# Kernel optimization log

Measured on AMD Instinct MI355X. Metric: run time of the kernel, lower is better.

Reference implementation:

```python
import jax, jax.numpy as jnp
import numpy as np

N_NODES = 100000
N_EDGES = 1600000
NODE_DIM = 64
EDGE_DIM = 32
HIDDEN = 64
LN_EPS = 1e-5


def _leaky_relu(x):
    return jnp.where(x >= 0, x, 0.1 * x)


def setup_inputs() -> dict:
    key = jax.random.key(0)
    ks = jax.random.split(key, 12)
    inp = {
        "node_features": jax.random.normal(ks[0], (N_NODES, NODE_DIM), dtype=jnp.float32),
        "edge_index": jax.random.randint(ks[1], (2, N_EDGES), 0, N_NODES, dtype=jnp.int32),
        "edge_attr": jax.random.normal(ks[2], (N_EDGES, EDGE_DIM), dtype=jnp.float32),
        "edge_weights": jax.random.uniform(ks[3], (N_EDGES,), dtype=jnp.float32),
        # message_mlp: Linear(node+edge -> hidden), LeakyReLU(0.1), Linear(hidden -> node)
        "mW1": jax.random.normal(ks[4], (NODE_DIM + EDGE_DIM, HIDDEN), dtype=jnp.float32) * 0.1,
        "mb1": jnp.zeros((HIDDEN,), dtype=jnp.float32),
        "mW2": jax.random.normal(ks[5], (HIDDEN, NODE_DIM), dtype=jnp.float32) * 0.1,
        "mb2": jnp.zeros((NODE_DIM,), dtype=jnp.float32),
        # update_mlp: Linear(2*node -> hidden), LayerNorm(hidden), LeakyReLU(0.1), Linear(hidden -> node)
        "uW1": jax.random.normal(ks[6], (2 * NODE_DIM, HIDDEN), dtype=jnp.float32) * 0.1,
        "ub1": jnp.zeros((HIDDEN,), dtype=jnp.float32),
        "ln_g": jnp.ones((HIDDEN,), dtype=jnp.float32),
        "ln_b": jnp.zeros((HIDDEN,), dtype=jnp.float32),
        "uW2": jax.random.normal(ks[7], (HIDDEN, NODE_DIM), dtype=jnp.float32) * 0.1,
        "ub2": jnp.zeros((NODE_DIM,), dtype=jnp.float32),
    }
    return inp


def reference(node_features, edge_index, edge_attr, edge_weights,
              mW1, mb1, mW2, mb2, uW1, ub1, ln_g, ln_b, uW2, ub2):
    src_idx, dst_idx = edge_index[0], edge_index[1]
    src_features = node_features[src_idx]                    # [E, node_dim] gather
    msg_input = jnp.concatenate([src_features, edge_attr], axis=-1)  # [E, node+edge]
    h = _leaky_relu(msg_input @ mW1 + mb1)                    # [E, hidden]
    messages = (h @ mW2 + mb2) * edge_weights[:, None]        # [E, node_dim]
    aggregated = jax.ops.segment_sum(messages, dst_idx, num_segments=node_features.shape[0])
    combined = jnp.concatenate([node_features, aggregated], axis=-1)  # [N, 2*node_dim]
    z = combined @ uW1 + ub1                                  # [N, hidden]
    mu = jnp.mean(z, axis=-1, keepdims=True)
    var = jnp.mean((z - mu) ** 2, axis=-1, keepdims=True)
    z = (z - mu) * jax.lax.rsqrt(var + LN_EPS) * ln_g + ln_b
    z = _leaky_relu(z)
    return z @ uW2 + ub2                                      # [N, node_dim]
```

## Files before the change

kernel.cpp:

```cpp
#include <hip/hip_runtime.h>
#include <cstdint>
#include <cstddef>

#define NN 100000
#define NE 1600000

typedef __attribute__((ext_vector_type(8))) short bf16x8;
typedef __attribute__((ext_vector_type(4))) short bf16x4;
typedef __attribute__((ext_vector_type(4))) float f32x4;

__device__ __forceinline__ short f2bf(float f) {
  uint32_t u = __builtin_bit_cast(uint32_t, f);
  u += 0x7FFFu + ((u >> 16) & 1u);
  return (short)(u >> 16);
}

__device__ __forceinline__ float lrelu(float x) { return fmaxf(x, 0.1f * x); }

__device__ __forceinline__ void atomic_add_f32(float* p, float v) {
  __hip_atomic_fetch_add(p, v, __ATOMIC_RELAXED, __HIP_MEMORY_SCOPE_AGENT);
}

__global__ void prep_kernel(const float* __restrict__ W1, const float* __restrict__ W2,
                            const float* __restrict__ uW1, const float* __restrict__ uW2,
                            short* __restrict__ ws) {
  int t = blockIdx.x * 256 + threadIdx.x;
  const int n1 = 64 * 96, n2 = 64 * 64, n3 = 64 * 128, n4 = 64 * 64;
  if (t < n1) { int c = t / 96, k = t % 96; ws[t] = f2bf(W1[k * 64 + c]); return; }
  t -= n1;
  if (t < n2) { int c = t / 64, k = t % 64; ws[n1 + t] = f2bf(W2[k * 64 + c]); return; }
  t -= n2;
  if (t < n3) { int c = t / 128, k = t % 128; ws[n1 + n2 + t] = f2bf(uW1[k * 64 + c]); return; }
  t -= n3;
  if (t < n4) { int c = t / 64, k = t % 64; ws[n1 + n2 + n3 + t] = f2bf(uW2[k * 64 + c]); return; }
}

__global__ __launch_bounds__(256) void edge_kernel(
    const float* __restrict__ nf, const int* __restrict__ ei,
    const float* __restrict__ ea, const float* __restrict__ ew,
    const short* __restrict__ W1t, const float* __restrict__ b1,
    const short* __restrict__ W2t, const float* __restrict__ b2,
    float* __restrict__ agg) {
  __shared__ uint4 hbuf_s[4][512];
  const int tid = threadIdx.x;
  const int wv = tid >> 6, ln = tid & 63;
  const int c = ln & 15, g = ln >> 4;
  char* hb = (char*)hbuf_s[wv];
  const long base = ((long)blockIdx.x * 4 + wv) * 64;

  int eid[4], srcn[4];
#pragma unroll
  for (int n = 0; n < 4; ++n) {
    eid[n] = (int)base + 16 * n + c;
    srcn[n] = ei[eid[n]];
  }

  f32x4 acc1[4][4];
#pragma unroll
  for (int i = 0; i < 4; ++i)
#pragma unroll
    for (int j = 0; j < 4; ++j) acc1[i][j] = f32x4{0.f, 0.f, 0.f, 0.f};

#pragma unroll
  for (int ks = 0; ks < 3; ++ks) {
    bf16x8 xf[4];
#pragma unroll
    for (int n = 0; n < 4; ++n) {
      const float* p = (ks < 2) ? (nf + (size_t)srcn[n] * 64 + ks * 32 + g * 8)
                                : (ea + (size_t)eid[n] * 32 + g * 8);
      float4 u = *(const float4*)p;
      float4 v = *(const float4*)(p + 4);
      bf16x8 t;
      t[0] = f2bf(u.x); t[1] = f2bf(u.y); t[2] = f2bf(u.z); t[3] = f2bf(u.w);
      t[4] = f2bf(v.x); t[5] = f2bf(v.y); t[6] = f2bf(v.z); t[7] = f2bf(v.w);
      xf[n] = t;
    }
#pragma unroll
    for (int m = 0; m < 4; ++m) {
      bf16x8 wf = *(const bf16x8*)(W1t + (size_t)(16 * m + c) * 96 + ks * 32 + g * 8);
#pragma unroll
      for (int n = 0; n < 4; ++n)
        acc1[m][n] = __builtin_amdgcn_mfma_f32_16x16x32_bf16(wf, xf[n], acc1[m][n], 0, 0, 0);
    }
  }

  float b1v[4][4];
#pragma unroll
  for (int m = 0; m < 4; ++m)
#pragma unroll
    for (int r = 0; r < 4; ++r) b1v[m][r] = b1[16 * m + 4 * g + r];

#pragma unroll
  for (int m = 0; m < 4; ++m) {
    const int h0 = 16 * m + 4 * g;
#pragma unroll
    for (int n = 0; n < 4; ++n) {
      const int e = 16 * n + c;
      bf16x4 pk;
#pragma unroll
      for (int r = 0; r < 4; ++r) pk[r] = f2bf(lrelu(acc1[m][n][r] + b1v[m][r]));
      const int byte = e * 128 + ((h0 * 2) ^ ((e & 7) << 4));
      *(bf16x4*)(hb + byte) = pk;
    }
  }

  f32x4 acc2[4][4];
#pragma unroll
  for (int i = 0; i < 4; ++i)
#pragma unroll
    for (int j = 0; j < 4; ++j) acc2[i][j] = f32x4{0.f, 0.f, 0.f, 0.f};

#pragma unroll
  for (int ks = 0; ks < 2; ++ks) {
    bf16x8 hf[4];
#pragma unroll
    for (int m = 0; m < 4; ++m) {
      const int e = 16 * m + c;
      const int byte = e * 128 + ((ks * 64 + g * 16) ^ ((e & 7) << 4));
      hf[m] = *(const bf16x8*)(hb + byte);
    }
#pragma unroll
    for (int n = 0; n < 4; ++n) {
      bf16x8 wf = *(const bf16x8*)(W2t + (size_t)(16 * n + c) * 64 + ks * 32 + g * 8);
#pragma unroll
      for (int m = 0; m < 4; ++m)
        acc2[m][n] = __builtin_amdgcn_mfma_f32_16x16x32_bf16(hf[m], wf, acc2[m][n], 0, 0, 0);
    }
  }

  float b2v[4];
#pragma unroll
  for (int n = 0; n < 4; ++n) b2v[n] = b2[16 * n + c];

#pragma unroll
  for (int m = 0; m < 4; ++m) {
#pragma unroll
    for (int r = 0; r < 4; ++r) {
      const long e = base + 16 * m + 4 * g + r;
      const float w = ew[e];
      const int dst = ei[NE + e];
      float* ab = agg + (size_t)dst * 64 + c;
#pragma unroll
      for (int n = 0; n < 4; ++n)
        atomic_add_f32(ab + 16 * n, (acc2[m][n][r] + b2v[n]) * w);
    }
  }
}

__global__ __launch_bounds__(256) void node_kernel(
    const float* __restrict__ nf,
    const short* __restrict__ W1t, const float* __restrict__ b1,
    const float* __restrict__ gam, const float* __restrict__ bet,
    const short* __restrict__ W2t, const float* __restrict__ b2,
    float* __restrict__ io) {
  __shared__ uint4 hbuf_s[4][512];
  const int tid = threadIdx.x;
  const int wv = tid >> 6, ln = tid & 63;
  const int c = ln & 15, g = ln >> 4;
  char* hb = (char*)hbuf_s[wv];
  const long base = ((long)blockIdx.x * 4 + wv) * 64;

  int nid[4];
#pragma unroll
  for (int n = 0; n < 4; ++n) {
    long r = base + 16 * n + c;
    nid[n] = (r < NN) ? (int)r : (NN - 1);
  }

  f32x4 acc1[4][4];
#pragma unroll
  for (int i = 0; i < 4; ++i)
#pragma unroll
    for (int j = 0; j < 4; ++j) acc1[i][j] = f32x4{0.f, 0.f, 0.f, 0.f};

#pragma unroll
  for (int ks = 0; ks < 4; ++ks) {
    bf16x8 xf[4];
#pragma unroll
    for (int n = 0; n < 4; ++n) {
      const float* p = (ks < 2) ? (nf + (size_t)nid[n] * 64 + ks * 32 + g * 8)
                                : (io + (size_t)nid[n] * 64 + (ks - 2) * 32 + g * 8);
      float4 u = *(const float4*)p;
      float4 v = *(const float4*)(p + 4);
      bf16x8 t;
      t[0] = f2bf(u.x); t[1] = f2bf(u.y); t[2] = f2bf(u.z); t[3] = f2bf(u.w);
      t[4] = f2bf(v.x); t[5] = f2bf(v.y); t[6] = f2bf(v.z); t[7] = f2bf(v.w);
      xf[n] = t;
    }
#pragma unroll
    for (int m = 0; m < 4; ++m) {
      bf16x8 wf = *(const bf16x8*)(W1t + (size_t)(16 * m + c) * 128 + ks * 32 + g * 8);
#pragma unroll
      for (int n = 0; n < 4; ++n)
        acc1[m][n] = __builtin_amdgcn_mfma_f32_16x16x32_bf16(wf, xf[n], acc1[m][n], 0, 0, 0);
    }
  }

  float b1v[4][4], gv[4][4], bv[4][4];
#pragma unroll
  for (int m = 0; m < 4; ++m)
#pragma unroll
    for (int r = 0; r < 4; ++r) {
      int h = 16 * m + 4 * g + r;
      b1v[m][r] = b1[h]; gv[m][r] = gam[h]; bv[m][r] = bet[h];
    }

#pragma unroll
  for (int n = 0; n < 4; ++n) {
    float s = 0.f;
#pragma unroll
    for (int m = 0; m < 4; ++m)
#pragma unroll
      for (int r = 0; r < 4; ++r) { acc1[m][n][r] += b1v[m][r]; s += acc1[m][n][r]; }
    s += __shfl_xor(s, 16);
    s += __shfl_xor(s, 32);
    const float mu = s * 0.015625f;
    float vs = 0.f;
#pragma unroll
    for (int m = 0; m < 4; ++m)
#pragma unroll
      for (int r = 0; r < 4; ++r) { float d = acc1[m][n][r] - mu; vs += d * d; }
    vs += __shfl_xor(vs, 16);
    vs += __shfl_xor(vs, 32);
    const float rstd = rsqrtf(vs * 0.015625f + 1e-5f);
    const int e = 16 * n + c;
#pragma unroll
    for (int m = 0; m < 4; ++m) {
      bf16x4 pk;
#pragma unroll
      for (int r = 0; r < 4; ++r)
        pk[r] = f2bf(lrelu((acc1[m][n][r] - mu) * rstd * gv[m][r] + bv[m][r]));
      const int byte = e * 128 + (((16 * m + 4 * g) * 2) ^ ((e & 7) << 4));
      *(bf16x4*)(hb + byte) = pk;
    }
  }

  f32x4 acc2[4][4];
#pragma unroll
  for (int i = 0; i < 4; ++i)
#pragma unroll
    for (int j = 0; j < 4; ++j) acc2[i][j] = f32x4{0.f, 0.f, 0.f, 0.f};

#pragma unroll
  for (int ks = 0; ks < 2; ++ks) {
    bf16x8 hf[4];
#pragma unroll
    for (int m = 0; m < 4; ++m) {
      const int e = 16 * m + c;
      const int byte = e * 128 + ((ks * 64 + g * 16) ^ ((e & 7) << 4));
      hf[m] = *(const bf16x8*)(hb + byte);
    }
#pragma unroll
    for (int n = 0; n < 4; ++n) {
      bf16x8 wf = *(const bf16x8*)(W2t + (size_t)(16 * n + c) * 64 + ks * 32 + g * 8);
#pragma unroll
      for (int m = 0; m < 4; ++m)
        acc2[m][n] = __builtin_amdgcn_mfma_f32_16x16x32_bf16(hf[m], wf, acc2[m][n], 0, 0, 0);
    }
  }

  float b2v[4];
#pragma unroll
  for (int n = 0; n < 4; ++n) b2v[n] = b2[16 * n + c];

#pragma unroll
  for (int m = 0; m < 4; ++m)
#pragma unroll
    for (int r = 0; r < 4; ++r) {
      const long node = base + 16 * m + 4 * g + r;
      if (node < NN) {
        float* op = io + (size_t)node * 64 + c;
#pragma unroll
        for (int n = 0; n < 4; ++n) op[16 * n] = acc2[m][n][r] + b2v[n];
      }
    }
}

extern "C" void kernel_launch(void* const* d_in, const int* in_sizes, int n_in,
                              void* d_out, int out_size, void* d_ws, size_t ws_size,
                              hipStream_t stream) {
  const float* nf  = (const float*)d_in[0];
  const int*   ei  = (const int*)d_in[1];
  const float* ea  = (const float*)d_in[2];
  const float* ew  = (const float*)d_in[3];
  const float* mW1 = (const float*)d_in[4];
  const float* mb1 = (const float*)d_in[5];
  const float* mW2 = (const float*)d_in[6];
  const float* mb2 = (const float*)d_in[7];
  const float* uW1 = (const float*)d_in[8];
  const float* ub1 = (const float*)d_in[9];
  const float* lng = (const float*)d_in[10];
  const float* lnb = (const float*)d_in[11];
  const float* uW2 = (const float*)d_in[12];
  const float* ub2 = (const float*)d_in[13];
  float* io = (float*)d_out;
  short* wsw = (short*)d_ws;

  hipMemsetAsync(d_out, 0, (size_t)NN * 64 * sizeof(float), stream);
  prep_kernel<<<88, 256, 0, stream>>>(mW1, mW2, uW1, uW2, wsw);

  const short* W1t  = wsw;
  const short* W2t  = wsw + 64 * 96;
  const short* uW1t = wsw + 64 * 96 + 64 * 64;
  const short* uW2t = uW1t + 64 * 128;

  edge_kernel<<<NE / 256, 256, 0, stream>>>(nf, ei, ea, ew, W1t, mb1, W2t, mb2, io);
  node_kernel<<<(NN + 255) / 256, 256, 0, stream>>>(nf, uW1t, ub1, lng, lnb, uW2t, ub2, io);
}
```

Baseline: 391.3 us.

## Sort edges by destination (CSR) and fuse edge MLP, aggregation and node update

Builds a destination-sorted edge list each call with a histogram, a two-level scan and an atomic scatter. A single fused kernel then processes 64 destination nodes per block: it runs the message MLP over that block's edges, accumulates into shared memory with LDS atomics instead of global atomics, and applies the update MLP with LayerNorm directly from shared memory. This removes the global atomic traffic, the output memset and the round trip of the aggregate through global memory. In exchange it adds several sort kernels and scattered writes, causes load imbalance across blocks with varying edge counts, and falls back to the old path if the workspace is too small.

New measurement: 950.6 us. +142.9%, slower.

```diff
diff --git a/kernel.cpp b/kernel.cpp
--- a/kernel.cpp
+++ b/kernel.cpp
@@ -4,10 +4,20 @@
 
 #define NN 100000
 #define NE 1600000
+#define NB ((NN + 63) / 64)
 
 typedef __attribute__((ext_vector_type(8))) short bf16x8;
 typedef __attribute__((ext_vector_type(4))) short bf16x4;
 typedef __attribute__((ext_vector_type(4))) float f32x4;
+
+#define OFF_W    0u
+#define OFF_CNT  45056u
+#define OFF_OFF  445056u
+#define OFF_CUR  845120u
+#define OFF_BS   1245120u
+#define OFF_SE   1245632u
+#define OFF_SD   14045632u
+#define WS_NEED  20445632u
 
 __device__ __forceinline__ short f2bf(float f) {
   uint32_t u = __builtin_bit_cast(uint32_t, f);
@@ -35,6 +45,300 @@
   if (t < n4) { int c = t / 64, k = t % 64; ws[n1 + n2 + n3 + t] = f2bf(uW2[k * 64 + c]); return; }
 }
 
+__global__ __launch_bounds__(256) void hist_kernel(const int* __restrict__ ei,
+                                                   int* __restrict__ cnt) {
+  int t = blockIdx.x * 256 + threadIdx.x;
+  if (t < NE) atomicAdd(&cnt[ei[NE + t]], 1);
+}
+
+__global__ __launch_bounds__(1024) void scan_block_kernel(const int* __restrict__ cnt,
+                                                          int* __restrict__ off,
+                                                          int* __restrict__ bs) {
+  __shared__ int wsum[16];
+  const int tid = threadIdx.x, lane = tid & 63, w = tid >> 6;
+  const int i = blockIdx.x * 1024 + tid;
+  int v = (i < NN) ? cnt[i] : 0;
+  int x = v;
+#pragma unroll
+  for (int d = 1; d < 64; d <<= 1) { int t = __shfl_up(x, d); if (lane >= d) x += t; }
+  if (lane == 63) wsum[w] = x;
+  __syncthreads();
+  if (w == 0) {
+    int s = (lane < 16) ? wsum[lane] : 0;
+#pragma unroll
+    for (int d = 1; d < 16; d <<= 1) { int t = __shfl_up(s, d); if (lane >= d) s += t; }
+    if (lane < 16) wsum[lane] = s;
+  }
+  __syncthreads();
+  int incl = x + ((w > 0) ? wsum[w - 1] : 0);
+  if (i < NN) off[i] = incl - v;
+  if (tid == 1023) bs[blockIdx.x] = incl;
+}
+
+__global__ __launch_bounds__(1024) void scan_add_kernel(int* __restrict__ off,
+                                                        const int* __restrict__ bs,
+                                                        int* __restrict__ cur) {
+  __shared__ int sbase;
+  const int tid = threadIdx.x, cB = blockIdx.x;
+  if (tid < 64) {
+    int s = 0;
+    if (tid < cB && tid < 98) s += bs[tid];
+    int j2 = tid + 64;
+    if (j2 < cB && j2 < 98) s += bs[j2];
+#pragma unroll
+    for (int d = 1; d < 64; d <<= 1) s += __shfl_xor(s, d);
+    if (tid == 0) sbase = s;
+  }
+  __syncthreads();
+  const int base = sbase;
+  const int i = cB * 1024 + tid;
+  if (i < NN) { int o = off[i] + base; off[i] = o; cur[i] = o; }
+}
+
+__global__ __launch_bounds__(256) void scatter_kernel(const int* __restrict__ ei,
+                                                      int* __restrict__ cur,
+                                                      int2* __restrict__ sse,
+                                                      int* __restrict__ sdst) {
+  int t = blockIdx.x * 256 + threadIdx.x;
+  if (t >= NE) return;
+  int d = ei[NE + t];
+  int pos = atomicAdd(&cur[d], 1);
+  sse[pos] = make_int2(ei[t], t);
+  sdst[pos] = d;
+}
+
+__global__ __launch_bounds__(256) void fused_kernel(
+    const float* __restrict__ nf, const float* __restrict__ ea,
+    const float* __restrict__ ew,
+    const int2* __restrict__ sse, const int* __restrict__ sdst,
+    const int* __restrict__ off,
+    const short* __restrict__ W1t, const float* __restrict__ b1,
+    const short* __restrict__ W2t, const float* __restrict__ b2,
+    const short* __restrict__ uW1t, const float* __restrict__ ub1,
+    const float* __restrict__ gam, const float* __restrict__ bet,
+    const short* __restrict__ uW2t, const float* __restrict__ ub2,
+    float* __restrict__ out) {
+  __shared__ float sAgg[64 * 68];
+  __shared__ uint4 hbuf_s[4][512];
+  __shared__ int   tdst[4][64];
+  __shared__ float tw[4][64];
+
+  const int tid = threadIdx.x;
+  const int wv = tid >> 6, ln = tid & 63;
+  const int c = ln & 15, g = ln >> 4;
+  char* hb = (char*)hbuf_s[wv];
+  const int nb = blockIdx.x * 64;
+
+  for (int i = tid; i < 64 * 68; i += 256) sAgg[i] = 0.f;
+
+  const int e0 = off[nb];
+  const int nhi = nb + 64;
+  const int e1 = (nhi >= NN) ? NE : off[nhi];
+  __syncthreads();
+
+  float b1v[4][4];
+#pragma unroll
+  for (int m = 0; m < 4; ++m)
+#pragma unroll
+    for (int r = 0; r < 4; ++r) b1v[m][r] = b1[16 * m + 4 * g + r];
+  float b2v[4];
+#pragma unroll
+  for (int n = 0; n < 4; ++n) b2v[n] = b2[16 * n + c];
+
+  for (int t0 = e0 + wv * 64; t0 < e1; t0 += 256) {
+    int src[4], eid[4];
+#pragma unroll
+    for (int n = 0; n < 4; ++n) {
+      int slot = t0 + 16 * n + c;
+      bool val = slot < e1;
+      int2 se = val ? sse[slot] : make_int2(0, 0);
+      src[n] = se.x; eid[n] = se.y;
+      if (g == 0) {
+        tdst[wv][16 * n + c] = val ? (sdst[slot] - nb) : 0;
+        tw[wv][16 * n + c]   = val ? ew[se.y] : 0.f;
+      }
+    }
+
+    f32x4 acc1[4][4];
+#pragma unroll
+    for (int i = 0; i < 4; ++i)
+#pragma unroll
+      for (int j = 0; j < 4; ++j) acc1[i][j] = f32x4{0.f, 0.f, 0.f, 0.f};
+
+#pragma unroll
+    for (int ks = 0; ks < 3; ++ks) {
+      bf16x8 xf[4];
+#pragma unroll
+      for (int n = 0; n < 4; ++n) {
+        const float* p = (ks < 2) ? (nf + (size_t)src[n] * 64 + ks * 32 + g * 8)
+                                  : (ea + (size_t)eid[n] * 32 + g * 8);
+        float4 u = *(const float4*)p;
+        float4 v = *(const float4*)(p + 4);
+        bf16x8 t;
+        t[0] = f2bf(u.x); t[1] = f2bf(u.y); t[2] = f2bf(u.z); t[3] = f2bf(u.w);
+        t[4] = f2bf(v.x); t[5] = f2bf(v.y); t[6] = f2bf(v.z); t[7] = f2bf(v.w);
+        xf[n] = t;
+      }
+#pragma unroll
+      for (int m = 0; m < 4; ++m) {
+        bf16x8 wf = *(const bf16x8*)(W1t + (size_t)(16 * m + c) * 96 + ks * 32 + g * 8);
+#pragma unroll
+        for (int n = 0; n < 4; ++n)
+          acc1[m][n] = __builtin_amdgcn_mfma_f32_16x16x32_bf16(wf, xf[n], acc1[m][n], 0, 0, 0);
+      }
+    }
+
+#pragma unroll
+    for (int m = 0; m < 4; ++m) {
+      const int h0 = 16 * m + 4 * g;
+#pragma unroll
+      for (int n = 0; n < 4; ++n) {
+        const int e = 16 * n + c;
+        bf16x4 pk;
+#pragma unroll
+        for (int r = 0; r < 4; ++r) pk[r] = f2bf(lrelu(acc1[m][n][r] + b1v[m][r]));
+        const int byte = e * 128 + ((h0 * 2) ^ ((e & 7) << 4));
+        *(bf16x4*)(hb + byte) = pk;
+      }
+    }
+
+    f32x4 acc2[4][4];
+#pragma unroll
+    for (int i = 0; i < 4; ++i)
+#pragma unroll
+      for (int j = 0; j < 4; ++j) acc2[i][j] = f32x4{0.f, 0.f, 0.f, 0.f};
+
+#pragma unroll
+    for (int ks = 0; ks < 2; ++ks) {
+      bf16x8 hf[4];
+#pragma unroll
+      for (int m = 0; m < 4; ++m) {
+        const int e = 16 * m + c;
+        const int byte = e * 128 + ((ks * 64 + g * 16) ^ ((e & 7) << 4));
+        hf[m] = *(const bf16x8*)(hb + byte);
+      }
+#pragma unroll
+      for (int n = 0; n < 4; ++n) {
+        bf16x8 wf = *(const bf16x8*)(W2t + (size_t)(16 * n + c) * 64 + ks * 32 + g * 8);
+#pragma unroll
+        for (int m = 0; m < 4; ++m)
+          acc2[m][n] = __builtin_amdgcn_mfma_f32_16x16x32_bf16(hf[m], wf, acc2[m][n], 0, 0, 0);
+      }
+    }
+
+#pragma unroll
+    for (int m = 0; m < 4; ++m)
+#pragma unroll
+      for (int r = 0; r < 4; ++r) {
+        const int s2 = 16 * m + 4 * g + r;
+        const int dl = tdst[wv][s2];
+        const float w = tw[wv][s2];
+#pragma unroll
+        for (int n = 0; n < 4; ++n)
+          atomicAdd(&sAgg[dl * 68 + c + 16 * n], (acc2[m][n][r] + b2v[n]) * w);
+      }
+  }
+  __syncthreads();
+
+  const int nloc = 16 * wv + c;
+  const int nodec = nb + nloc;
+  const int ncl = (nodec < NN) ? nodec : (NN - 1);
+
+  f32x4 un[4];
+#pragma unroll
+  for (int m = 0; m < 4; ++m) un[m] = f32x4{0.f, 0.f, 0.f, 0.f};
+
+#pragma unroll
+  for (int ks = 0; ks < 4; ++ks) {
+    bf16x8 xf;
+    float4 u, v;
+    if (ks < 2) {
+      const float* p = nf + (size_t)ncl * 64 + ks * 32 + g * 8;
+      u = *(const float4*)p; v = *(const float4*)(p + 4);
+    } else {
+      const float* p = sAgg + nloc * 68 + (ks - 2) * 32 + g * 8;
+      u = *(const float4*)p; v = *(const float4*)(p + 4);
+    }
+    xf[0] = f2bf(u.x); xf[1] = f2bf(u.y); xf[2] = f2bf(u.z); xf[3] = f2bf(u.w);
+    xf[4] = f2bf(v.x); xf[5] = f2bf(v.y); xf[6] = f2bf(v.z); xf[7] = f2bf(v.w);
+#pragma unroll
+    for (int m = 0; m < 4; ++m) {
+      bf16x8 wf = *(const bf16x8*)(uW1t + (size_t)(16 * m + c) * 128 + ks * 32 + g * 8);
+      un[m] = __builtin_amdgcn_mfma_f32_16x16x32_bf16(wf, xf, un[m], 0, 0, 0);
+    }
+  }
+
+  float b1n[4][4], gn[4][4], bn[4][4];
+#pragma unroll
+  for (int m = 0; m < 4; ++m)
+#pragma unroll
+    for (int r = 0; r < 4; ++r) {
+      int h = 16 * m + 4 * g + r;
+      b1n[m][r] = ub1[h]; gn[m][r] = gam[h]; bn[m][r] = bet[h];
+    }
+
+  float s = 0.f;
+#pragma unroll
+  for (int m = 0; m < 4; ++m)
+#pragma unroll
+    for (int r = 0; r < 4; ++r) { un[m][r] += b1n[m][r]; s += un[m][r]; }
+  s += __shfl_xor(s, 16);
+  s += __shfl_xor(s, 32);
+  const float mu = s * 0.015625f;
+  float vs = 0.f;
+#pragma unroll
+  for (int m = 0; m < 4; ++m)
+#pragma unroll
+    for (int r = 0; r < 4; ++r) { float d = un[m][r] - mu; vs += d * d; }
+  vs += __shfl_xor(vs, 16);
+  vs += __shfl_xor(vs, 32);
+  const float rstd = rsqrtf(vs * 0.015625f + 1e-5f);
+
+  bf16x4 pk[4];
+#pragma unroll
+  for (int m = 0; m < 4; ++m)
+#pragma unroll
+    for (int r = 0; r < 4; ++r)
+      pk[m][r] = f2bf(lrelu((un[m][r] - mu) * rstd * gn[m][r] + bn[m][r]));
+
+  __syncthreads();
+  char* hb2 = (char*)sAgg;
+#pragma unroll
+  for (int m = 0; m < 4; ++m) {
+    const int h0 = 16 * m + 4 * g;
+    const int byte = nloc * 128 + ((h0 * 2) ^ ((nloc & 7) << 4));
+    *(bf16x4*)(hb2 + byte) = pk[m];
+  }
+  __syncthreads();
+
+  f32x4 ac[4];
+#pragma unroll
+  for (int n = 0; n < 4; ++n) ac[n] = f32x4{0.f, 0.f, 0.f, 0.f};
+#pragma unroll
+  for (int ks = 0; ks < 2; ++ks) {
+    const int byte = nloc * 128 + ((ks * 64 + g * 16) ^ ((nloc & 7) << 4));
+    bf16x8 hf = *(const bf16x8*)(hb2 + byte);
+#pragma unroll
+    for (int n = 0; n < 4; ++n) {
+      bf16x8 wf = *(const bf16x8*)(uW2t + (size_t)(16 * n + c) * 64 + ks * 32 + g * 8);
+      ac[n] = __builtin_amdgcn_mfma_f32_16x16x32_bf16(hf, wf, ac[n], 0, 0, 0);
+    }
+  }
+
+  float b2n[4];
+#pragma unroll
+  for (int n = 0; n < 4; ++n) b2n[n] = ub2[16 * n + c];
+#pragma unroll
+  for (int r = 0; r < 4; ++r) {
+    const int node = nb + 16 * wv + 4 * g + r;
+    if (node < NN) {
+      float* op = out + (size_t)node * 64 + c;
+#pragma unroll
+      for (int n = 0; n < 4; ++n) op[16 * n] = ac[n][r] + b2n[n];
+    }
+  }
+}
+
 __global__ __launch_bounds__(256) void edge_kernel(
     const float* __restrict__ nf, const int* __restrict__ ei,
     const float* __restrict__ ea, const float* __restrict__ ew,
@@ -54,13 +358,11 @@
     eid[n] = (int)base + 16 * n + c;
     srcn[n] = ei[eid[n]];
   }
-
   f32x4 acc1[4][4];
 #pragma unroll
   for (int i = 0; i < 4; ++i)
 #pragma unroll
     for (int j = 0; j < 4; ++j) acc1[i][j] = f32x4{0.f, 0.f, 0.f, 0.f};
-
 #pragma unroll
   for (int ks = 0; ks < 3; ++ks) {
     bf16x8 xf[4];
@@ -83,13 +385,11 @@
         acc1[m][n] = __builtin_amdgcn_mfma_f32_16x16x32_bf16(wf, xf[n], acc1[m][n], 0, 0, 0);
     }
   }
-
   float b1v[4][4];
 #pragma unroll
   for (int m = 0; m < 4; ++m)
 #pragma unroll
     for (int r = 0; r < 4; ++r) b1v[m][r] = b1[16 * m + 4 * g + r];
-
 #pragma unroll
   for (int m = 0; m < 4; ++m) {
     const int h0 = 16 * m + 4 * g;
@@ -103,13 +403,11 @@
       *(bf16x4*)(hb + byte) = pk;
     }
   }
-
   f32x4 acc2[4][4];
 #pragma unroll
   for (int i = 0; i < 4; ++i)
 #pragma unroll
     for (int j = 0; j < 4; ++j) acc2[i][j] = f32x4{0.f, 0.f, 0.f, 0.f};
-
 #pragma unroll
   for (int ks = 0; ks < 2; ++ks) {
     bf16x8 hf[4];
@@ -127,13 +425,11 @@
         acc2[m][n] = __builtin_amdgcn_mfma_f32_16x16x32_bf16(hf[m], wf, acc2[m][n], 0, 0, 0);
     }
   }
-
   float b2v[4];
 #pragma unroll
   for (int n = 0; n < 4; ++n) b2v[n] = b2[16 * n + c];
-
-#pragma unroll
-  for (int m = 0; m < 4; ++m) {
+#pragma unroll
+  for (int m = 0; m < 4; ++m)
 #pragma unroll
     for (int r = 0; r < 4; ++r) {
       const long e = base + 16 * m + 4 * g + r;
@@ -144,7 +440,6 @@
       for (int n = 0; n < 4; ++n)
         atomic_add_f32(ab + 16 * n, (acc2[m][n][r] + b2v[n]) * w);
     }
-  }
 }
 
 __global__ __launch_bounds__(256) void node_kernel(
@@ -166,13 +461,11 @@
     long r = base + 16 * n + c;
     nid[n] = (r < NN) ? (int)r : (NN - 1);
   }
-
   f32x4 acc1[4][4];
 #pragma unroll
   for (int i = 0; i < 4; ++i)
 #pragma unroll
     for (int j = 0; j < 4; ++j) acc1[i][j] = f32x4{0.f, 0.f, 0.f, 0.f};
-
 #pragma unroll
   for (int ks = 0; ks < 4; ++ks) {
     bf16x8 xf[4];
@@ -195,7 +488,6 @@
         acc1[m][n] = __builtin_amdgcn_mfma_f32_16x16x32_bf16(wf, xf[n], acc1[m][n], 0, 0, 0);
     }
   }
-
   float b1v[4][4], gv[4][4], bv[4][4];
 #pragma unroll
   for (int m = 0; m < 4; ++m)
@@ -204,7 +496,6 @@
       int h = 16 * m + 4 * g + r;
       b1v[m][r] = b1[h]; gv[m][r] = gam[h]; bv[m][r] = bet[h];
     }
-
 #pragma unroll
   for (int n = 0; n < 4; ++n) {
     float s = 0.f;
@@ -234,13 +525,11 @@
       *(bf16x4*)(hb + byte) = pk;
     }
   }
-
   f32x4 acc2[4][4];
 #pragma unroll
   for (int i = 0; i < 4; ++i)
 #pragma unroll
     for (int j = 0; j < 4; ++j) acc2[i][j] = f32x4{0.f, 0.f, 0.f, 0.f};
-
 #pragma unroll
   for (int ks = 0; ks < 2; ++ks) {
     bf16x8 hf[4];
@@ -258,11 +547,9 @@
         acc2[m][n] = __builtin_amdgcn_mfma_f32_16x16x32_bf16(hf[m], wf, acc2[m][n], 0, 0, 0);
     }
   }
-
   float b2v[4];
 #pragma unroll
   for (int n = 0; n < 4; ++n) b2v[n] = b2[16 * n + c];
-
 #pragma unroll
   for (int m = 0; m < 4; ++m)
 #pragma unroll
@@ -294,16 +581,34 @@
   const float* uW2 = (const float*)d_in[12];
   const float* ub2 = (const float*)d_in[13];
   float* io = (float*)d_out;
-  short* wsw = (short*)d_ws;
-
-  hipMemsetAsync(d_out, 0, (size_t)NN * 64 * sizeof(float), stream);
-  prep_kernel<<<88, 256, 0, stream>>>(mW1, mW2, uW1, uW2, wsw);
-
-  const short* W1t  = wsw;
-  const short* W2t  = wsw + 64 * 96;
-  const short* uW1t = wsw + 64 * 96 + 64 * 64;
+  char* ws = (char*)d_ws;
+
+  short* Wall = (short*)(ws + OFF_W);
+  prep_kernel<<<88, 256, 0, stream>>>(mW1, mW2, uW1, uW2, Wall);
+  const short* W1t  = Wall;
+  const short* W2t  = Wall + 64 * 96;
+  const short* uW1t = Wall + 64 * 96 + 64 * 64;
   const short* uW2t = uW1t + 64 * 128;
 
-  edge_kernel<<<NE / 256, 256, 0, stream>>>(nf, ei, ea, ew, W1t, mb1, W2t, mb2, io);
-  node_kernel<<<(NN + 255) / 256, 256, 0, stream>>>(nf, uW1t, ub1, lng, lnb, uW2t, ub2, io);
-}
+  if (ws_size >= (size_t)WS_NEED) {
+    int*  cnt  = (int*)(ws + OFF_CNT);
+    int*  off  = (int*)(ws + OFF_OFF);
+    int*  cur  = (int*)(ws + OFF_CUR);
+    int*  bs   = (int*)(ws + OFF_BS);
+    int2* sse  = (int2*)(ws + OFF_SE);
+    int*  sdst = (int*)(ws + OFF_SD);
+
+    hipMemsetAsync(cnt, 0, (size_t)NN * sizeof(int), stream);
+    hist_kernel<<<NE / 256, 256, 0, stream>>>(ei, cnt);
+    scan_block_kernel<<<98, 1024, 0, stream>>>(cnt, off, bs);
+    scan_add_kernel<<<98, 1024, 0, stream>>>(off, bs, cur);
+    scatter_kernel<<<NE / 256, 256, 0, stream>>>(ei, cur, sse, sdst);
+    fused_kernel<<<NB, 256, 0, stream>>>(nf, ea, ew, sse, sdst, off,
+                                         W1t, mb1, W2t, mb2,
+                                         uW1t, ub1, lng, lnb, uW2t, ub2, io);
+  } else {
+    hipMemsetAsync(d_out, 0, (size_t)NN * 64 * sizeof(float), stream);
+    edge_kernel<<<NE / 256, 256, 0, stream>>>(nf, ei, ea, ew, W1t, mb1, W2t, mb2, io);
+    node_kernel<<<(NN + 255) / 256, 256, 0, stream>>>(nf, uW1t, ub1, lng, lnb, uW2t, ub2, io);
+  }
+}
```
